# Kernel optimization log

Hardware: AMD Instinct MI355X
Metric: run time of the kernel (lower is better)

## Reference

```python
import jax, jax.numpy as jnp
import numpy as np

N = 20000
E = 320000
NEG_SLOPE = 0.2
BN_EPS = 1e-5


def _segment_softmax(e, dst, n):
    # e: [E, H] attention logits, dst: [E] destination node ids
    m = jax.ops.segment_max(e, dst, num_segments=n)           # [N, H]
    ex = jnp.exp(e - m[dst])                                   # [E, H]
    s = jax.ops.segment_sum(ex, dst, num_segments=n)          # [N, H]
    return ex / s[dst]


def gat_conv(x, src, dst, W, a_src, a_dst, b, heads, out_ch):
    # PyG GATConv (concat=True): h = x @ W reshaped to [N, H, C]
    n = x.shape[0]
    h = (x @ W).reshape(n, heads, out_ch)                      # [N, H, C]
    al_s = jnp.einsum('nhc,hc->nh', h, a_src)                  # [N, H]
    al_d = jnp.einsum('nhc,hc->nh', h, a_dst)
    e = jax.nn.leaky_relu(al_s[src] + al_d[dst], NEG_SLOPE)    # [E, H]
    alpha = _segment_softmax(e, dst, n)                        # [E, H]
    msg = h[src] * alpha[:, :, None]                           # [E, H, C]
    out = jax.ops.segment_sum(msg, dst, num_segments=n)        # [N, H, C]
    return out.reshape(n, heads * out_ch) + b


def batch_norm(x, gamma, beta):
    mu = jnp.mean(x, axis=0)
    var = jnp.mean((x - mu) ** 2, axis=0)  # biased, as torch BN training
    return gamma * (x - mu) * jax.lax.rsqrt(var + BN_EPS) + beta


def setup_inputs() -> dict:
    key = jax.random.key(0)
    ks = jax.random.split(key, 16)
    F_in, H1, C1 = 128, 8, 64
    D = H1 * C1  # 512
    OUT = 2
    def gl(k, shape, fan):
        return jax.random.normal(k, shape, dtype=jnp.float32) / np.sqrt(fan)
    x = jax.random.normal(ks[0], (N, F_in), dtype=jnp.float32)
    edge_index = jax.random.randint(ks[1], (2, E), 0, N, dtype=jnp.int64)
    return {
        'x': x, 'edge_index': edge_index,
        'W1': gl(ks[2], (F_in, H1 * C1), F_in),
        'a1s': gl(ks[3], (H1, C1), C1), 'a1d': gl(ks[4], (H1, C1), C1),
        'b1': jnp.zeros((D,), jnp.float32),
        'W2': gl(ks[5], (D, D), D),
        'a2s': gl(ks[6], (1, D), D), 'a2d': gl(ks[7], (1, D), D),
        'b2': jnp.zeros((D,), jnp.float32),
        'fc1_w': gl(ks[8], (D, D), D), 'fc1_b': jnp.zeros((D,), jnp.float32),
        'g1': jnp.ones((D,), jnp.float32), 'be1': jnp.zeros((D,), jnp.float32),
        'fc2_w': gl(ks[9], (D, D), D), 'fc2_b': jnp.zeros((D,), jnp.float32),
        'g2': jnp.ones((D,), jnp.float32), 'be2': jnp.zeros((D,), jnp.float32),
        'lin_w': gl(ks[10], (D, OUT), D), 'lin_b': jnp.zeros((OUT,), jnp.float32),
    }


def reference(x, edge_index, W1, a1s, a1d, b1, W2, a2s, a2d, b2,
              fc1_w, fc1_b, g1, be1, fc2_w, fc2_b, g2, be2, lin_w, lin_b):
    n = x.shape[0]
    loop = jnp.arange(n, dtype=edge_index.dtype)
    src = jnp.concatenate([edge_index[0], loop])  # add self-loops (PyG default)
    dst = jnp.concatenate([edge_index[1], loop])
    h = gat_conv(x, src, dst, W1, a1s, a1d, b1, heads=8, out_ch=64)
    h = batch_norm(jax.nn.relu(h @ fc1_w + fc1_b), g1, be1)
    h = gat_conv(h, src, dst, W2, a2s, a2d, b2, heads=1, out_ch=512)
    h = batch_norm(jax.nn.relu(h @ fc2_w + fc2_b), g2, be2)
    out = jax.nn.relu(h @ lin_w + lin_b)  # dropout p=0 is identity
    return out
```

## Files before the change

kernel.cpp:

```cpp
#include <hip/hip_runtime.h>
#include <hip/hip_bf16.h>

static constexpr int NN = 20000;
static constexpr int EE = 320000;
static constexpr int ET = EE + NN;
static constexpr int DD = 512;
static constexpr int FIN = 128;

typedef __attribute__((ext_vector_type(8))) short short8;
typedef __attribute__((ext_vector_type(4))) float f32x4;

__device__ __forceinline__ unsigned short f2bf(float f) {
    unsigned u = __float_as_uint(f);
    u += 0x7fffu + ((u >> 16) & 1u);
    return (unsigned short)(u >> 16);
}
__device__ __forceinline__ float bf2f(unsigned short b) {
    return __uint_as_float(((unsigned)b) << 16);
}

__device__ __forceinline__ void async_copy16(short* lds, const unsigned short* g) {
    __builtin_amdgcn_global_load_lds(
        (const __attribute__((address_space(1))) unsigned int*)g,
        (__attribute__((address_space(3))) unsigned int*)lds,
        16, 0, 0);
}

template <int IS64>
__global__ void count_deg(const void* __restrict__ ei, int* __restrict__ deg) {
    int i = blockIdx.x * blockDim.x + threadIdx.x;
    if (i >= EE) return;
    int d = IS64 ? (int)((const long long*)ei)[EE + i] : ((const int*)ei)[EE + i];
    atomicAdd(&deg[d], 1);
}

__global__ void scan_k(const int* __restrict__ deg, int* __restrict__ row_ptr) {
    __shared__ int part[1024];
    int t = threadIdx.x;
    const int CH = (NN + 1023) / 1024;
    int start = t * CH;
    int end = min(start + CH, NN);
    int s = 0;
    for (int i = start; i < end; ++i) s += deg[i] + 1;
    part[t] = s;
    __syncthreads();
    for (int off = 1; off < 1024; off <<= 1) {
        int v = 0;
        if (t >= off) v = part[t - off];
        __syncthreads();
        part[t] += v;
        __syncthreads();
    }
    int base = (t == 0) ? 0 : part[t - 1];
    for (int i = start; i < end; ++i) { row_ptr[i] = base; base += deg[i] + 1; }
    if (t == 1023) row_ptr[NN] = part[1023];
}

template <int IS64>
__global__ void fill_csr(const void* __restrict__ ei,
                         const int* __restrict__ row_ptr, int* __restrict__ cursor,
                         int* __restrict__ csr_src, int* __restrict__ csr_dst) {
    int e = blockIdx.x * blockDim.x + threadIdx.x;
    if (e >= ET) return;
    int s, d;
    if (e < EE) {
        if (IS64) {
            const long long* p = (const long long*)ei;
            s = (int)p[e]; d = (int)p[EE + e];
        } else {
            const int* p = (const int*)ei;
            s = p[e]; d = p[EE + e];
        }
    } else {
        s = d = e - EE;
    }
    int pos = atomicAdd(&cursor[d], 1);
    int slot = row_ptr[d] + pos;
    csr_src[slot] = s;
    csr_dst[slot] = d;
}

static constexpr int TBLK = 208;
static constexpr int SZ_X4 = NN * FIN / 4;
__global__ __launch_bounds__(256) void prep_all_k(
    const float* __restrict__ x, const float* __restrict__ W1,
    const float* __restrict__ fc1, const float* __restrict__ W2,
    const float* __restrict__ fc2,
    unsigned short* __restrict__ xb, unsigned short* __restrict__ W1t,
    unsigned short* __restrict__ fc1t, unsigned short* __restrict__ W2t,
    unsigned short* __restrict__ fc2t) {
    int b = blockIdx.x;
    if (b < TBLK) {
        __shared__ unsigned short tile[64][65];
        const float* src; unsigned short* dst; int rows, cols;
        if (b < 16)       { src = W1;  dst = W1t;  rows = FIN; cols = DD; }
        else if (b < 80)  { b -= 16;  src = fc1; dst = fc1t; rows = DD; cols = DD; }
        else if (b < 144) { b -= 80;  src = W2;  dst = W2t;  rows = DD; cols = DD; }
        else              { b -= 144; src = fc2; dst = fc2t; rows = DD; cols = DD; }
        int tc = cols / 64;
        int r0 = (b / tc) * 64, c0 = (b % tc) * 64;
        int t = threadIdx.x, lr = t >> 6, lc = t & 63;
#pragma unroll
        for (int p = 0; p < 16; ++p) {
            int r = lr + p * 4;
            tile[r][lc] = f2bf(src[(size_t)(r0 + r) * cols + c0 + lc]);
        }
        __syncthreads();
#pragma unroll
        for (int p = 0; p < 16; ++p) {
            int r = lr + p * 4;
            dst[(size_t)(c0 + r) * rows + r0 + lc] = tile[lc][r];
        }
        return;
    }
    int i = (b - TBLK) * 256 + threadIdx.x;
    if (i < SZ_X4) {
        float4 v = ((const float4*)x)[i];
        unsigned short o[4] = {f2bf(v.x), f2bf(v.y), f2bf(v.z), f2bf(v.w)};
        *(unsigned long long*)(xb + (size_t)i * 4) = *(const unsigned long long*)o;
    }
}

template <int RELU, int HASBIAS, int STATS, int ALS, int H>
__global__ __launch_bounds__(256) void gemm_bf16(const unsigned short* __restrict__ A,
                                                 const unsigned short* __restrict__ Bt,
                                                 const float* __restrict__ bias,
                                                 unsigned short* __restrict__ Cb,
                                                 float* __restrict__ bnstat,
                                                 const float* __restrict__ avs,
                                                 const float* __restrict__ avd,
                                                 float* __restrict__ al_s,
                                                 float* __restrict__ al_d,
                                                 int M, int Nc, int K) {
    int id = blockIdx.x;
    int bm = ((id >> 5) << 3) + (id & 7);
    int bn = (id >> 3) & 3;
    int m0 = bm * 128, n0 = bn * 128;
    if (m0 >= M) return;

    __shared__ short As0[128 * 32], As1[128 * 32];
    __shared__ short Bs0[128 * 32], Bs1[128 * 32];
    int t = threadIdx.x;
    int lane = t & 63, w = t >> 6;
    int wm = w & 1, wn = w >> 1;
    int quad = lane >> 4, mr = lane & 15;
    int lrow = lane >> 2;
    int lcol = (lane & 3) * 8;

    const unsigned short* Ag0 = A + (size_t)(m0 + w * 32 + lrow) * K + lcol;
    const unsigned short* Ag1 = A + (size_t)(m0 + w * 32 + 16 + lrow) * K + lcol;
    const unsigned short* Bg0 = Bt + (size_t)(n0 + w * 32 + lrow) * K + lcol;
    const unsigned short* Bg1 = Bt + (size_t)(n0 + w * 32 + 16 + lrow) * K + lcol;
    short* Al[2][2] = {{&As0[(w * 32) * 32], &As0[(w * 32 + 16) * 32]},
                       {&As1[(w * 32) * 32], &As1[(w * 32 + 16) * 32]}};
    short* Bl[2][2] = {{&Bs0[(w * 32) * 32], &Bs0[(w * 32 + 16) * 32]},
                       {&Bs1[(w * 32) * 32], &Bs1[(w * 32 + 16) * 32]}};

    f32x4 zero = {0.f, 0.f, 0.f, 0.f};
    f32x4 acc[4][4];
#pragma unroll
    for (int i = 0; i < 4; ++i)
#pragma unroll
        for (int j = 0; j < 4; ++j) acc[i][j] = zero;

    for (int k0 = 0; k0 < K; k0 += 64) {
        async_copy16(Al[0][0], Ag0 + k0);
        async_copy16(Al[1][0], Ag0 + k0 + 32);
        async_copy16(Al[0][1], Ag1 + k0);
        async_copy16(Al[1][1], Ag1 + k0 + 32);
        async_copy16(Bl[0][0], Bg0 + k0);
        async_copy16(Bl[1][0], Bg0 + k0 + 32);
        async_copy16(Bl[0][1], Bg1 + k0);
        async_copy16(Bl[1][1], Bg1 + k0 + 32);
        __syncthreads();
#pragma unroll
        for (int kp = 0; kp < 2; ++kp) {
            const short* Sa = kp ? As1 : As0;
            const short* Sb = kp ? Bs1 : Bs0;
            short8 af[4], bfr[4];
#pragma unroll
            for (int i = 0; i < 4; ++i) {
                af[i]  = *(const short8*)(&Sa[(wm * 64 + i * 16 + mr) * 32 + quad * 8]);
                bfr[i] = *(const short8*)(&Sb[(wn * 64 + i * 16 + mr) * 32 + quad * 8]);
            }
#pragma unroll
            for (int i = 0; i < 4; ++i)
#pragma unroll
                for (int j = 0; j < 4; ++j)
                    acc[i][j] = __builtin_amdgcn_mfma_f32_16x16x32_bf16(af[i], bfr[j], acc[i][j], 0, 0, 0);
        }
        __syncthreads();
    }

    float as_j[4], ad_j[4];
    if (ALS) {
#pragma unroll
        for (int j = 0; j < 4; ++j) {
            int n = n0 + wn * 64 + j * 16 + mr;
            as_j[j] = avs[n];
            ad_j[j] = avd[n];
        }
    }
    const int head = (H == 8) ? ((n0 + wn * 64) >> 6) : 0;
    float sj[4] = {0.f, 0.f, 0.f, 0.f}, qj[4] = {0.f, 0.f, 0.f, 0.f};
#pragma unroll
    for (int i = 0; i < 4; ++i) {
        int mb = m0 + wm * 64 + i * 16 + quad * 4;
#pragma unroll
        for (int r = 0; r < 4; ++r) {
            int m = mb + r;
            bool valid = (m < M);
            float ps = 0.f, pd = 0.f;
#pragma unroll
            for (int j = 0; j < 4; ++j) {
                int n = n0 + wn * 64 + j * 16 + mr;
                float v = acc[i][j][r];
                if (HASBIAS) v += bias[n];
                if (RELU) v = fmaxf(v, 0.f);
                unsigned short hb = f2bf(v);
                if (valid) Cb[(size_t)m * Nc + n] = hb;
                if (ALS) {
                    float vv = bf2f(hb);
                    ps += as_j[j] * vv;
                    pd += ad_j[j] * vv;
                }
                if (STATS && valid) { sj[j] += v; qj[j] += v * v; }
            }
            if (ALS) {
                ps += __shfl_xor(ps, 1); pd += __shfl_xor(pd, 1);
                ps += __shfl_xor(ps, 2); pd += __shfl_xor(pd, 2);
                ps += __shfl_xor(ps, 4); pd += __shfl_xor(pd, 4);
                ps += __shfl_xor(ps, 8); pd += __shfl_xor(pd, 8);
                if (mr == 0 && valid) {
                    if (H == 8) { al_s[m * 8 + head] = ps; al_d[m * 8 + head] = pd; }
                    else        { atomicAdd(&al_s[m], ps); atomicAdd(&al_d[m], pd); }
                }
            }
        }
    }
    if (STATS) {
#pragma unroll
        for (int j = 0; j < 4; ++j) {
            float s = sj[j], q = qj[j];
            s += __shfl_xor(s, 16); q += __shfl_xor(q, 16);
            s += __shfl_xor(s, 32); q += __shfl_xor(q, 32);
            if (lane < 16) {
                int n = n0 + wn * 64 + j * 16 + mr;
                atomicAdd(&bnstat[n], s);
                atomicAdd(&bnstat[512 + n], q);
            }
        }
    }
}

__global__ __launch_bounds__(256) void alpha1_k(const float* __restrict__ al_s,
                                                const float* __restrict__ al_d,
                                                const int* __restrict__ csr_src,
                                                const int* __restrict__ csr_dst,
                                                int2* __restrict__ ea) {
    int p = blockIdx.x * blockDim.x + threadIdx.x;
    if (p >= ET) return;
    int sn = csr_src[p], d = csr_dst[p];
    float4 s0 = *(const float4*)(al_s + (size_t)sn * 8);
    float4 s1 = *(const float4*)(al_s + (size_t)sn * 8 + 4);
    float4 d0 = *(const float4*)(al_d + (size_t)d * 8);
    float4 d1 = *(const float4*)(al_d + (size_t)d * 8 + 4);
    float l[8] = {s0.x + d0.x, s0.y + d0.y, s0.z + d0.z, s0.w + d0.w,
                  s1.x + d1.x, s1.y + d1.y, s1.z + d1.z, s1.w + d1.w};
#pragma unroll
    for (int h = 0; h < 8; ++h) {
        float xx = l[h];
        float a = __expf((xx > 0.f) ? xx : 0.2f * xx);
        ea[(size_t)h * ET + p] = make_int2(sn, __float_as_int(a));
    }
}

__global__ __launch_bounds__(256) void alpha2_k(const float* __restrict__ al_s,
                                                const float* __restrict__ al_d,
                                                const int* __restrict__ csr_src,
                                                const int* __restrict__ csr_dst,
                                                int2* __restrict__ ea) {
    int p = blockIdx.x * blockDim.x + threadIdx.x;
    if (p >= ET) return;
    int sn = csr_src[p], d = csr_dst[p];
    float xx = al_s[sn] + al_d[d];
    float a = __expf((xx > 0.f) ? xx : 0.2f * xx);
    ea[p] = make_int2(sn, __float_as_int(a));
}

template <int H>
__global__ __launch_bounds__(256) void gat_gather_k(const unsigned short* __restrict__ hb,
                                                    const int2* __restrict__ ea,
                                                    const int* __restrict__ row_ptr,
                                                    const float* __restrict__ bias,
                                                    unsigned short* __restrict__ outb) {
    int b = blockIdx.x;
    int s = b & 7;
    int g = b >> 3;
    int t = threadIdx.x;
    int w = t >> 6, lane = t & 63;
    int grp = lane >> 3, cg = lane & 7;
    int n = g * 32 + w * 8 + grp;
    int col = s * 64 + cg * 8;
    const int2* ep = ea + (H == 8 ? (size_t)s * ET : (size_t)0);
    const char* hbase = (const char*)hb + col * 2;
    int beg = row_ptr[n], end = row_ptr[n + 1];

    float acc[8] = {0.f, 0.f, 0.f, 0.f, 0.f, 0.f, 0.f, 0.f};
    float psum = 0.f;
    int p = beg;
    for (; p + 4 <= end; p += 4) {
        int2 v0 = ep[p], v1 = ep[p + 1], v2 = ep[p + 2], v3 = ep[p + 3];
        short8 h0 = *(const short8*)(hbase + ((unsigned)v0.x << 10));
        short8 h1 = *(const short8*)(hbase + ((unsigned)v1.x << 10));
        short8 h2 = *(const short8*)(hbase + ((unsigned)v2.x << 10));
        short8 h3 = *(const short8*)(hbase + ((unsigned)v3.x << 10));
        float a0 = __int_as_float(v0.y), a1 = __int_as_float(v1.y);
        float a2 = __int_as_float(v2.y), a3 = __int_as_float(v3.y);
        psum += a0 + a1 + a2 + a3;
#pragma unroll
        for (int j = 0; j < 8; ++j) {
            acc[j] = fmaf(a0, bf2f((unsigned short)h0[j]), acc[j]);
            acc[j] = fmaf(a1, bf2f((unsigned short)h1[j]), acc[j]);
            acc[j] = fmaf(a2, bf2f((unsigned short)h2[j]), acc[j]);
            acc[j] = fmaf(a3, bf2f((unsigned short)h3[j]), acc[j]);
        }
    }
    for (; p < end; ++p) {
        int2 v = ep[p];
        float a = __int_as_float(v.y);
        psum += a;
        short8 hv = *(const short8*)(hbase + ((unsigned)v.x << 10));
#pragma unroll
        for (int j = 0; j < 8; ++j)
            acc[j] = fmaf(a, bf2f((unsigned short)hv[j]), acc[j]);
    }
    float inv = 1.0f / psum;
    unsigned short ov[8];
#pragma unroll
    for (int j = 0; j < 8; ++j) ov[j] = f2bf(acc[j] * inv + bias[col + j]);
    *(int4*)(outb + (size_t)n * DD + col) = *(const int4*)ov;
}

__global__ __launch_bounds__(256) void fold1_k(const float* __restrict__ stat,
                                               const float* __restrict__ g,
                                               const float* __restrict__ be,
                                               unsigned short* __restrict__ W2t,
                                               float* __restrict__ bias2) {
    int t = threadIdx.x;
    int n = blockIdx.x * 4 + (t >> 6);
    int lane = t & 63;
    float pb = 0.f;
#pragma unroll
    for (int j = 0; j < 8; ++j) {
        int k = lane * 8 + j;
        float mean = stat[k] * (1.0f / NN);
        float var = stat[512 + k] * (1.0f / NN) - mean * mean;
        float sc = g[k] * rsqrtf(var + 1e-5f);
        float sh = be[k] - mean * sc;
        float wv = bf2f(W2t[n * DD + k]);
        W2t[n * DD + k] = f2bf(sc * wv);
        pb += sh * wv;
    }
    for (int off = 32; off; off >>= 1) pb += __shfl_down(pb, off);
    if (lane == 0) bias2[n] = pb;
}

__global__ void final_linear(const unsigned short* __restrict__ xb,
                             const float* __restrict__ stat, const float* __restrict__ g,
                             const float* __restrict__ be, const float* __restrict__ w,
                             const float* __restrict__ b, float* __restrict__ out) {
    int wave = (blockIdx.x * blockDim.x + threadIdx.x) >> 6;
    int lane = threadIdx.x & 63;
    if (wave >= NN) return;
    short8 hv = *(const short8*)(xb + (size_t)wave * DD + lane * 8);
    float p0 = 0.f, p1 = 0.f;
#pragma unroll
    for (int j = 0; j < 8; ++j) {
        int c = lane * 8 + j;
        float mean = stat[c] * (1.0f / NN);
        float var = stat[512 + c] * (1.0f / NN) - mean * mean;
        float sc = g[c] * rsqrtf(var + 1e-5f);
        float vn = (bf2f((unsigned short)hv[j]) - mean) * sc + be[c];
        p0 += vn * w[2 * c];
        p1 += vn * w[2 * c + 1];
    }
    for (int off = 32; off; off >>= 1) {
        p0 += __shfl_down(p0, off);
        p1 += __shfl_down(p1, off);
    }
    if (lane == 0) {
        out[wave * 2 + 0] = fmaxf(p0 + b[0], 0.f);
        out[wave * 2 + 1] = fmaxf(p1 + b[1], 0.f);
    }
}

extern "C" void kernel_launch(void* const* d_in, const int* in_sizes, int n_in,
                              void* d_out, int out_size, void* d_ws, size_t ws_size,
                              hipStream_t stream) {
    const float* x     = (const float*)d_in[0];
    const void*  ei    = d_in[1];
    const float* W1    = (const float*)d_in[2];
    const float* a1s   = (const float*)d_in[3];
    const float* a1d   = (const float*)d_in[4];
    const float* b1    = (const float*)d_in[5];
    const float* W2    = (const float*)d_in[6];
    const float* a2s   = (const float*)d_in[7];
    const float* a2d   = (const float*)d_in[8];
    const float* b2    = (const float*)d_in[9];
    const float* fc1_w = (const float*)d_in[10];
    const float* fc1_b = (const float*)d_in[11];
    const float* g1    = (const float*)d_in[12];
    const float* be1   = (const float*)d_in[13];
    const float* fc2_w = (const float*)d_in[14];
    const float* fc2_b = (const float*)d_in[15];
    const float* g2    = (const float*)d_in[16];
    const float* be2   = (const float*)d_in[17];
    const float* lin_w = (const float*)d_in[18];
    const float* lin_b = (const float*)d_in[19];
    float* out = (float*)d_out;

    char* ws = (char*)d_ws;
    auto alloc = [&](size_t bytes) {
        void* p = (void*)ws;
        ws += (bytes + 255) & ~size_t(255);
        return p;
    };
    unsigned short* h_bf    = (unsigned short*)alloc((size_t)NN * DD * 2);
    unsigned short* act_bf  = (unsigned short*)alloc((size_t)NN * DD * 2);
    unsigned short* W1t     = (unsigned short*)alloc((size_t)DD * FIN * 2);
    unsigned short* fc1t    = (unsigned short*)alloc((size_t)DD * DD * 2);
    unsigned short* W2t     = (unsigned short*)alloc((size_t)DD * DD * 2);
    unsigned short* fc2t    = (unsigned short*)alloc((size_t)DD * DD * 2);
    float*          al_s    = (float*)alloc((size_t)NN * 8 * 4);
    float*          al_d    = (float*)alloc((size_t)NN * 8 * 4);
    int*            row_ptr = (int*)alloc((size_t)(NN + 1) * 4);
    int*            csr_src = (int*)alloc((size_t)ET * 4);
    int*            csr_dst = (int*)alloc((size_t)ET * 4);
    float*          bias2f  = (float*)alloc(512 * 4);
    int2*           ea      = (int2*)alloc((size_t)8 * ET * 8);
    int*            deg     = (int*)alloc((size_t)2 * NN * 4);
    int*            cursor  = deg + NN;
    float*          bnstatA = (float*)alloc((size_t)(2048 + 2 * NN) * 4);
    float*          bnstatB = bnstatA + 1024;
    float*          al_s2   = bnstatA + 2048;
    float*          al_d2   = al_s2 + NN;

    const int is64 = (in_sizes[1] >= (int)(2u * EE * 8u)) ? 1 : 0;

    hipMemsetAsync(deg, 0, (size_t)2 * NN * 4, stream);
    hipMemsetAsync(bnstatA, 0, (size_t)(2048 + 2 * NN) * 4, stream);

    if (is64) {
        count_deg<1><<<(EE + 255) / 256, 256, 0, stream>>>(ei, deg);
    } else {
        count_deg<0><<<(EE + 255) / 256, 256, 0, stream>>>(ei, deg);
    }
    scan_k<<<1, 1024, 0, stream>>>(deg, row_ptr);
    if (is64) {
        fill_csr<1><<<(ET + 255) / 256, 256, 0, stream>>>(ei, row_ptr, cursor, csr_src, csr_dst);
    } else {
        fill_csr<0><<<(ET + 255) / 256, 256, 0, stream>>>(ei, row_ptr, cursor, csr_src, csr_dst);
    }

    unsigned short* x_bf = act_bf;
    const int prep_blocks = TBLK + (SZ_X4 + 255) / 256;
    prep_all_k<<<prep_blocks, 256, 0, stream>>>(x, W1, fc1_w, W2, fc2_w,
                                                x_bf, W1t, fc1t, W2t, fc2t);

    const int GB = 640;
    const int GGB = 8 * (NN / 32);
    const int AB = (ET + 255) / 256;

    gemm_bf16<0, 0, 0, 1, 8><<<GB, 256, 0, stream>>>(
        x_bf, W1t, nullptr, h_bf, nullptr, a1s, a1d, al_s, al_d, NN, DD, FIN);
    alpha1_k<<<AB, 256, 0, stream>>>(al_s, al_d, csr_src, csr_dst, ea);
    gat_gather_k<8><<<GGB, 256, 0, stream>>>(h_bf, ea, row_ptr, b1, act_bf);
    gemm_bf16<1, 1, 1, 0, 8><<<GB, 256, 0, stream>>>(
        act_bf, fc1t, fc1_b, h_bf, bnstatA, nullptr, nullptr, nullptr, nullptr, NN, DD, DD);
    fold1_k<<<128, 256, 0, stream>>>(bnstatA, g1, be1, W2t, bias2f);

    gemm_bf16<0, 1, 0, 1, 1><<<GB, 256, 0, stream>>>(
        h_bf, W2t, bias2f, act_bf, nullptr, a2s, a2d, al_s2, al_d2, NN, DD, DD);
    alpha2_k<<<AB, 256, 0, stream>>>(al_s2, al_d2, csr_src, csr_dst, ea);
    gat_gather_k<1><<<GGB, 256, 0, stream>>>(act_bf, ea, row_ptr, b2, h_bf);
    gemm_bf16<1, 1, 1, 0, 8><<<GB, 256, 0, stream>>>(
        h_bf, fc2t, fc2_b, act_bf, bnstatB, nullptr, nullptr, nullptr, nullptr, NN, DD, DD);

    final_linear<<<(NN + 3) / 4, 256, 0, stream>>>(act_bf, bnstatB, g2, be2, lin_w, lin_b, out);
}
```

Before: 352.3 us.

## Fuse CSR build into prep/GEMM kernels and degree-sort gather rows

Degree counting is folded into the prep kernel, and CSR fill runs as extra blocks appended to the first GEMM launch, which removes separate launches. The scan kernel also builds a degree-bucketed permutation so the gather kernel handles nodes in descending degree order, balancing work across wavefronts. The gather inner loop is rewritten to process 8 edges per step, with the next batch of edge records software-prefetched and padding entries masked out. This trades some extra single-block work in the scan, and scattered node order in the gather, for fewer launches and better load balance and latency hiding.

```diff
diff --git a/kernel.cpp b/kernel.cpp
--- a/kernel.cpp
+++ b/kernel.cpp
@@ -26,22 +26,23 @@
         16, 0, 0);
 }
 
-template <int IS64>
-__global__ void count_deg(const void* __restrict__ ei, int* __restrict__ deg) {
-    int i = blockIdx.x * blockDim.x + threadIdx.x;
-    if (i >= EE) return;
-    int d = IS64 ? (int)((const long long*)ei)[EE + i] : ((const int*)ei)[EE + i];
-    atomicAdd(&deg[d], 1);
-}
-
-__global__ void scan_k(const int* __restrict__ deg, int* __restrict__ row_ptr) {
+__global__ void scan_k(const int* __restrict__ deg, int* __restrict__ row_ptr,
+                       int* __restrict__ perm) {
     __shared__ int part[1024];
+    __shared__ int hist[512];
+    __shared__ int hbase[512];
     int t = threadIdx.x;
+    if (t < 512) hist[t] = 0;
+    __syncthreads();
     const int CH = (NN + 1023) / 1024;
     int start = t * CH;
     int end = min(start + CH, NN);
     int s = 0;
-    for (int i = start; i < end; ++i) s += deg[i] + 1;
+    for (int i = start; i < end; ++i) {
+        int d = deg[i] + 1;
+        s += d;
+        atomicAdd(&hist[min(d, 511)], 1);
+    }
     part[t] = s;
     __syncthreads();
     for (int off = 1; off < 1024; off <<= 1) {
@@ -54,42 +55,40 @@
     int base = (t == 0) ? 0 : part[t - 1];
     for (int i = start; i < end; ++i) { row_ptr[i] = base; base += deg[i] + 1; }
     if (t == 1023) row_ptr[NN] = part[1023];
-}
-
-template <int IS64>
-__global__ void fill_csr(const void* __restrict__ ei,
-                         const int* __restrict__ row_ptr, int* __restrict__ cursor,
-                         int* __restrict__ csr_src, int* __restrict__ csr_dst) {
-    int e = blockIdx.x * blockDim.x + threadIdx.x;
-    if (e >= ET) return;
-    int s, d;
-    if (e < EE) {
-        if (IS64) {
-            const long long* p = (const long long*)ei;
-            s = (int)p[e]; d = (int)p[EE + e];
-        } else {
-            const int* p = (const int*)ei;
-            s = p[e]; d = p[EE + e];
-        }
-    } else {
-        s = d = e - EE;
-    }
-    int pos = atomicAdd(&cursor[d], 1);
-    int slot = row_ptr[d] + pos;
-    csr_src[slot] = s;
-    csr_dst[slot] = d;
+    if (t == 0) {
+        int a = 0;
+        for (int b2 = 0; b2 < 512; ++b2) { hbase[b2] = a; a += hist[b2]; }
+    }
+    __syncthreads();
+    for (int i = start; i < end; ++i) {
+        int d = min(deg[i] + 1, 511);
+        int pos = atomicAdd(&hbase[d], 1);
+        perm[NN - 1 - pos] = i;
+    }
 }
 
 static constexpr int TBLK = 208;
 static constexpr int SZ_X4 = NN * FIN / 4;
+static constexpr int XCB = (SZ_X4 + 255) / 256;
+static constexpr int CDB = (EE + 255) / 256;
 __global__ __launch_bounds__(256) void prep_all_k(
     const float* __restrict__ x, const float* __restrict__ W1,
     const float* __restrict__ fc1, const float* __restrict__ W2,
     const float* __restrict__ fc2,
     unsigned short* __restrict__ xb, unsigned short* __restrict__ W1t,
     unsigned short* __restrict__ fc1t, unsigned short* __restrict__ W2t,
-    unsigned short* __restrict__ fc2t) {
+    unsigned short* __restrict__ fc2t,
+    const void* __restrict__ ei, int is64, int* __restrict__ deg) {
     int b = blockIdx.x;
+    if (b < CDB) {
+        int i = b * 256 + threadIdx.x;
+        if (i < EE) {
+            int d = is64 ? (int)((const long long*)ei)[EE + i] : ((const int*)ei)[EE + i];
+            atomicAdd(&deg[d], 1);
+        }
+        return;
+    }
+    b -= CDB;
     if (b < TBLK) {
         __shared__ unsigned short tile[64][65];
         const float* src; unsigned short* dst; int rows, cols;
@@ -121,7 +120,7 @@
     }
 }
 
-template <int RELU, int HASBIAS, int STATS, int ALS, int H>
+template <int RELU, int HASBIAS, int STATS, int ALS, int H, int FILLEX>
 __global__ __launch_bounds__(256) void gemm_bf16(const unsigned short* __restrict__ A,
                                                  const unsigned short* __restrict__ Bt,
                                                  const float* __restrict__ bias,
@@ -131,8 +130,34 @@
                                                  const float* __restrict__ avd,
                                                  float* __restrict__ al_s,
                                                  float* __restrict__ al_d,
-                                                 int M, int Nc, int K) {
+                                                 int M, int Nc, int K,
+                                                 const void* __restrict__ ei, int is64,
+                                                 const int* __restrict__ rp,
+                                                 int* __restrict__ cursor,
+                                                 int* __restrict__ csr_src,
+                                                 int* __restrict__ csr_dst) {
     int id = blockIdx.x;
+    if (FILLEX && id >= 640) {
+        int e = (id - 640) * 256 + threadIdx.x;
+        if (e >= ET) return;
+        int s, d;
+        if (e < EE) {
+            if (is64) {
+                const long long* p = (const long long*)ei;
+                s = (int)p[e]; d = (int)p[EE + e];
+            } else {
+                const int* p = (const int*)ei;
+                s = p[e]; d = p[EE + e];
+            }
+        } else {
+            s = d = e - EE;
+        }
+        int pos = atomicAdd(&cursor[d], 1);
+        int slot = rp[d] + pos;
+        csr_src[slot] = s;
+        csr_dst[slot] = d;
+        return;
+    }
     int bm = ((id >> 5) << 3) + (id & 7);
     int bn = (id >> 3) & 3;
     int m0 = bm * 128, n0 = bn * 128;
@@ -292,6 +317,7 @@
 __global__ __launch_bounds__(256) void gat_gather_k(const unsigned short* __restrict__ hb,
                                                     const int2* __restrict__ ea,
                                                     const int* __restrict__ row_ptr,
+                                                    const int* __restrict__ perm,
                                                     const float* __restrict__ bias,
                                                     unsigned short* __restrict__ outb) {
     int b = blockIdx.x;
@@ -300,40 +326,54 @@
     int t = threadIdx.x;
     int w = t >> 6, lane = t & 63;
     int grp = lane >> 3, cg = lane & 7;
-    int n = g * 32 + w * 8 + grp;
+    int n = perm[g * 32 + w * 8 + grp];
     int col = s * 64 + cg * 8;
     const int2* ep = ea + (H == 8 ? (size_t)s * ET : (size_t)0);
     const char* hbase = (const char*)hb + col * 2;
     int beg = row_ptr[n], end = row_ptr[n + 1];
+    int last = end - 1;
+    int nb = (end - beg + 7) >> 3;
 
     float acc[8] = {0.f, 0.f, 0.f, 0.f, 0.f, 0.f, 0.f, 0.f};
     float psum = 0.f;
-    int p = beg;
-    for (; p + 4 <= end; p += 4) {
-        int2 v0 = ep[p], v1 = ep[p + 1], v2 = ep[p + 2], v3 = ep[p + 3];
-        short8 h0 = *(const short8*)(hbase + ((unsigned)v0.x << 10));
-        short8 h1 = *(const short8*)(hbase + ((unsigned)v1.x << 10));
-        short8 h2 = *(const short8*)(hbase + ((unsigned)v2.x << 10));
-        short8 h3 = *(const short8*)(hbase + ((unsigned)v3.x << 10));
-        float a0 = __int_as_float(v0.y), a1 = __int_as_float(v1.y);
-        float a2 = __int_as_float(v2.y), a3 = __int_as_float(v3.y);
-        psum += a0 + a1 + a2 + a3;
-#pragma unroll
-        for (int j = 0; j < 8; ++j) {
-            acc[j] = fmaf(a0, bf2f((unsigned short)h0[j]), acc[j]);
-            acc[j] = fmaf(a1, bf2f((unsigned short)h1[j]), acc[j]);
-            acc[j] = fmaf(a2, bf2f((unsigned short)h2[j]), acc[j]);
-            acc[j] = fmaf(a3, bf2f((unsigned short)h3[j]), acc[j]);
-        }
-    }
-    for (; p < end; ++p) {
-        int2 v = ep[p];
-        float a = __int_as_float(v.y);
-        psum += a;
-        short8 hv = *(const short8*)(hbase + ((unsigned)v.x << 10));
-#pragma unroll
-        for (int j = 0; j < 8; ++j)
-            acc[j] = fmaf(a, bf2f((unsigned short)hv[j]), acc[j]);
+    int2 v[8];
+#pragma unroll
+    for (int u = 0; u < 8; ++u) {
+        int pp = beg + u;
+        int2 r = ep[min(pp, last)];
+        if (pp > last) r.y = 0;
+        v[u] = r;
+    }
+    for (int bb = 1; bb <= nb; ++bb) {
+        short8 hreg[8];
+#pragma unroll
+        for (int u = 0; u < 8; ++u)
+            hreg[u] = *(const short8*)(hbase + ((unsigned)v[u].x << 10));
+        float av[8];
+#pragma unroll
+        for (int u = 0; u < 8; ++u) av[u] = __int_as_float(v[u].y);
+        int2 vn[8];
+        if (bb < nb) {
+            int p0 = beg + bb * 8;
+#pragma unroll
+            for (int u = 0; u < 8; ++u) {
+                int pp = p0 + u;
+                int2 r = ep[min(pp, last)];
+                if (pp > last) r.y = 0;
+                vn[u] = r;
+            }
+        }
+#pragma unroll
+        for (int u = 0; u < 8; ++u) psum += av[u];
+#pragma unroll
+        for (int u = 0; u < 8; ++u)
+#pragma unroll
+            for (int j = 0; j < 8; ++j)
+                acc[j] = fmaf(av[u], bf2f((unsigned short)hreg[u][j]), acc[j]);
+        if (bb < nb) {
+#pragma unroll
+            for (int u = 0; u < 8; ++u) v[u] = vn[u];
+        }
     }
     float inv = 1.0f / psum;
     unsigned short ov[8];
@@ -437,6 +477,7 @@
     int*            row_ptr = (int*)alloc((size_t)(NN + 1) * 4);
     int*            csr_src = (int*)alloc((size_t)ET * 4);
     int*            csr_dst = (int*)alloc((size_t)ET * 4);
+    int*            perm    = (int*)alloc((size_t)NN * 4);
     float*          bias2f  = (float*)alloc(512 * 4);
     int2*           ea      = (int2*)alloc((size_t)8 * ET * 8);
     int*            deg     = (int*)alloc((size_t)2 * NN * 4);
@@ -451,41 +492,36 @@
     hipMemsetAsync(deg, 0, (size_t)2 * NN * 4, stream);
     hipMemsetAsync(bnstatA, 0, (size_t)(2048 + 2 * NN) * 4, stream);
 
-    if (is64) {
-        count_deg<1><<<(EE + 255) / 256, 256, 0, stream>>>(ei, deg);
-    } else {
-        count_deg<0><<<(EE + 255) / 256, 256, 0, stream>>>(ei, deg);
-    }
-    scan_k<<<1, 1024, 0, stream>>>(deg, row_ptr);
-    if (is64) {
-        fill_csr<1><<<(ET + 255) / 256, 256, 0, stream>>>(ei, row_ptr, cursor, csr_src, csr_dst);
-    } else {
-        fill_csr<0><<<(ET + 255) / 256, 256, 0, stream>>>(ei, row_ptr, cursor, csr_src, csr_dst);
-    }
-
     unsigned short* x_bf = act_bf;
-    const int prep_blocks = TBLK + (SZ_X4 + 255) / 256;
+    const int prep_blocks = CDB + TBLK + XCB;
     prep_all_k<<<prep_blocks, 256, 0, stream>>>(x, W1, fc1_w, W2, fc2_w,
-                                                x_bf, W1t, fc1t, W2t, fc2t);
+                                                x_bf, W1t, fc1t, W2t, fc2t,
+                                                ei, is64, deg);
+    scan_k<<<1, 1024, 0, stream>>>(deg, row_ptr, perm);
 
     const int GB = 640;
+    const int FB = (ET + 255) / 256;
     const int GGB = 8 * (NN / 32);
     const int AB = (ET + 255) / 256;
 
-    gemm_bf16<0, 0, 0, 1, 8><<<GB, 256, 0, stream>>>(
-        x_bf, W1t, nullptr, h_bf, nullptr, a1s, a1d, al_s, al_d, NN, DD, FIN);
+    gemm_bf16<0, 0, 0, 1, 8, 1><<<GB + FB, 256, 0, stream>>>(
+        x_bf, W1t, nullptr, h_bf, nullptr, a1s, a1d, al_s, al_d, NN, DD, FIN,
+        ei, is64, row_ptr, cursor, csr_src, csr_dst);
     alpha1_k<<<AB, 256, 0, stream>>>(al_s, al_d, csr_src, csr_dst, ea);
-    gat_gather_k<8><<<GGB, 256, 0, stream>>>(h_bf, ea, row_ptr, b1, act_bf);
-    gemm_bf16<1, 1, 1, 0, 8><<<GB, 256, 0, stream>>>(
-        act_bf, fc1t, fc1_b, h_bf, bnstatA, nullptr, nullptr, nullptr, nullptr, NN, DD, DD);
+    gat_gather_k<8><<<GGB, 256, 0, stream>>>(h_bf, ea, row_ptr, perm, b1, act_bf);
+    gemm_bf16<1, 1, 1, 0, 8, 0><<<GB, 256, 0, stream>>>(
+        act_bf, fc1t, fc1_b, h_bf, bnstatA, nullptr, nullptr, nullptr, nullptr, NN, DD, DD,
+        nullptr, 0, nullptr, nullptr, nullptr, nullptr);
     fold1_k<<<128, 256, 0, stream>>>(bnstatA, g1, be1, W2t, bias2f);
 
-    gemm_bf16<0, 1, 0, 1, 1><<<GB, 256, 0, stream>>>(
-        h_bf, W2t, bias2f, act_bf, nullptr, a2s, a2d, al_s2, al_d2, NN, DD, DD);
+    gemm_bf16<0, 1, 0, 1, 1, 0><<<GB, 256, 0, stream>>>(
+        h_bf, W2t, bias2f, act_bf, nullptr, a2s, a2d, al_s2, al_d2, NN, DD, DD,
+        nullptr, 0, nullptr, nullptr, nullptr, nullptr);
     alpha2_k<<<AB, 256, 0, stream>>>(al_s2, al_d2, csr_src, csr_dst, ea);
-    gat_gather_k<1><<<GGB, 256, 0, stream>>>(act_bf, ea, row_ptr, b2, h_bf);
-    gemm_bf16<1, 1, 1, 0, 8><<<GB, 256, 0, stream>>>(
-        h_bf, fc2t, fc2_b, act_bf, bnstatB, nullptr, nullptr, nullptr, nullptr, NN, DD, DD);
+    gat_gather_k<1><<<GGB, 256, 0, stream>>>(act_bf, ea, row_ptr, perm, b2, h_bf);
+    gemm_bf16<1, 1, 1, 0, 8, 0><<<GB, 256, 0, stream>>>(
+        h_bf, fc2t, fc2_b, act_bf, bnstatB, nullptr, nullptr, nullptr, nullptr, NN, DD, DD,
+        nullptr, 0, nullptr, nullptr, nullptr, nullptr);
 
     final_linear<<<(NN + 3) / 4, 256, 0, stream>>>(act_bf, bnstatB, g2, be2, lin_w, lin_b, out);
 }
```

Result: no change. 358.7 us (+1.8%).
